# Kernel optimization log

Measured on AMD Instinct MI355X. Metric: run time of the kernel, lower is better.

The kernel has to match this reference:

```python
import jax, jax.numpy as jnp
import numpy as np

N_NODES = 50000
N_EDGES = 1600000
N_GRAPHS = 512
IN_DIM = 384
HID = 128


def gcn_conv(x, W, b, src, dst, n_nodes):
    # PyG GCNConv: h = W^T x, then propagate with sym norm over A + I (self-loops).
    h = x @ W  # [N, out]
    # self-loops
    loop = jnp.arange(n_nodes, dtype=src.dtype)
    s = jnp.concatenate([src, loop])
    d = jnp.concatenate([dst, loop])
    ones = jnp.ones(s.shape[0], dtype=h.dtype)
    deg = jax.ops.segment_sum(ones, d, num_segments=n_nodes)  # in-degree incl self-loop
    dis = jnp.where(deg > 0, jax.lax.rsqrt(deg), 0.0)
    norm = dis[s] * dis[d]  # [E+N]
    msg = h[s] * norm[:, None]  # gather + scale
    out = jax.ops.segment_sum(msg, d, num_segments=n_nodes)  # scatter-add
    return out + b


def global_mean_pool(x, batch, num_graphs):
    sums = jax.ops.segment_sum(x, batch, num_segments=num_graphs)
    cnt = jax.ops.segment_sum(jnp.ones(x.shape[0], dtype=x.dtype), batch, num_segments=num_graphs)
    return sums / jnp.maximum(cnt, 1.0)[:, None]


def setup_inputs() -> dict:
    key = jax.random.key(0)
    ks = jax.random.split(key, 12)
    x = jax.random.normal(ks[0], (N_NODES, IN_DIM), dtype=jnp.float32)
    edge_index = jax.random.randint(ks[1], (2, N_EDGES), 0, N_NODES, dtype=jnp.int64 if jax.config.jax_enable_x64 else jnp.int32)
    batch = jnp.sort(jax.random.randint(ks[2], (N_NODES,), 0, N_GRAPHS, dtype=jnp.int32))
    def glorot(k, shape):
        lim = float(np.sqrt(6.0 / (shape[0] + shape[1])))
        return jax.random.uniform(k, shape, jnp.float32, -lim, lim)
    return {
        "x": x,
        "edge_index": edge_index,
        "batch": batch,
        "W1": glorot(ks[3], (IN_DIM, HID)),
        "b1": jnp.zeros((HID,), jnp.float32),
        "W2": glorot(ks[4], (HID, HID)),
        "b2": jnp.zeros((HID,), jnp.float32),
        "Wl1": glorot(ks[5], (HID, HID // 2)),
        "bl1": jnp.zeros((HID // 2,), jnp.float32),
        "Wl2": glorot(ks[6], (HID // 2, 5)),
        "bl2": jnp.zeros((5,), jnp.float32),
    }


def reference(x, edge_index, batch, W1, b1, W2, b2, Wl1, bl1, Wl2, bl2):
    src, dst = edge_index[0], edge_index[1]
    n = x.shape[0]
    h = jax.nn.relu(gcn_conv(x, W1, b1, src, dst, n))
    h = jax.nn.relu(gcn_conv(h, W2, b2, src, dst, n))
    g = global_mean_pool(h, batch, N_GRAPHS)  # [G, HID]
    g = jax.nn.relu(g @ Wl1 + bl1)
    return jax.nn.sigmoid(g @ Wl2 + bl2)  # [G, 5]
```

## Files before the change

kernel.cpp:

```cpp
#include <hip/hip_runtime.h>
#include <hip/hip_bf16.h>
#include <string.h>

#define HID 128
#define NGRAPH 512
#define IN_DIM 384

typedef __attribute__((ext_vector_type(2))) float f32x2;

__device__ __forceinline__ float bf2f(unsigned short u) {
    unsigned int x = ((unsigned int)u) << 16;
    float f; __builtin_memcpy(&f, &x, 4); return f;
}
__device__ __forceinline__ unsigned short f2bf(float f) {
    unsigned int b; __builtin_memcpy(&b, &f, 4);
    unsigned int r = (b + 0x7FFFu + ((b >> 16) & 1u)) >> 16;
    return (unsigned short)r;
}

__global__ void deg_kernel(const int* __restrict__ dst, int* __restrict__ deg, int E) {
    int e = blockIdx.x * blockDim.x + threadIdx.x;
    if (e < E) atomicAdd(&deg[dst[e]], 1);
}

__global__ void dis_kernel(const int* __restrict__ deg, float* __restrict__ dis, int n) {
    int v = blockIdx.x * blockDim.x + threadIdx.x;
    if (v < n) dis[v] = rsqrtf((float)(deg[v] + 1));
}

__global__ __launch_bounds__(256) void scan_part(const int* __restrict__ deg, int* __restrict__ row,
                                                 int* __restrict__ blockSums, int n) {
    __shared__ int ts[256];
    const int b = blockIdx.x, t = threadIdx.x;
    const int base = b * 1024 + t * 4;
    int v0 = (base + 0 < n) ? deg[base + 0] : 0;
    int v1 = (base + 1 < n) ? deg[base + 1] : 0;
    int v2 = (base + 2 < n) ? deg[base + 2] : 0;
    int v3 = (base + 3 < n) ? deg[base + 3] : 0;
    const int s = v0 + v1 + v2 + v3;
    ts[t] = s;
    __syncthreads();
    for (int off = 1; off < 256; off <<= 1) {
        int x = (t >= off) ? ts[t - off] : 0;
        __syncthreads();
        ts[t] += x;
        __syncthreads();
    }
    int p = ts[t] - s;
    if (base + 0 < n) { row[base + 0] = p; p += v0; }
    if (base + 1 < n) { row[base + 1] = p; p += v1; }
    if (base + 2 < n) { row[base + 2] = p; p += v2; }
    if (base + 3 < n) { row[base + 3] = p; }
    if (t == 255) blockSums[b] = ts[255];
}

__global__ void scan_tops(int* __restrict__ blockSums, int nb) {
    if (threadIdx.x == 0 && blockIdx.x == 0) {
        int acc = 0;
        for (int i = 0; i < nb; i++) { int v = blockSums[i]; blockSums[i] = acc; acc += v; }
    }
}

__global__ __launch_bounds__(256) void scan_add(int* __restrict__ row, int* __restrict__ cursor,
                                                const int* __restrict__ blockSums, int n, int E) {
    const int b = blockIdx.x, t = threadIdx.x;
    const int off = blockSums[b];
    const int base = b * 1024 + t * 4;
#pragma unroll
    for (int j = 0; j < 4; j++) {
        int i = base + j;
        if (i < n) { int v = row[i] + off; row[i] = v; cursor[i] = v; }
    }
    if (b == 0 && t == 0) row[n] = E;
}

__global__ void fill_kernel(const int* __restrict__ src, const int* __restrict__ dst,
                            int* __restrict__ cursor, unsigned short* __restrict__ csr16,
                            int E, int lo, int hi) {
    int e = blockIdx.x * blockDim.x + threadIdx.x;
    if (e < E) {
        const int d = dst[e];
        if (d >= lo && d < hi) {
            int pos = atomicAdd(&cursor[d], 1);
            csr16[pos] = (unsigned short)src[e];
        }
    }
}

template <int K, bool BF16IN>
__global__ __launch_bounds__(256) void gemm_tile(const void* __restrict__ Xv,
                                                 const float* __restrict__ W,
                                                 const float* __restrict__ dis,
                                                 unsigned int* __restrict__ out8, int n) {
    constexpr int KC = 32;
    __shared__ float asT[KC][68];
    __shared__ float bs[KC * HID];
    const int t = threadIdx.x;
    const int tx = t & 31;
    const int ty = t >> 5;
    const int row0 = blockIdx.x * 64;

    float4 acc[8];
#pragma unroll
    for (int j = 0; j < 8; j++) acc[j] = make_float4(0.f, 0.f, 0.f, 0.f);

    const int ar = t >> 3;
    const int af = t & 7;

    for (int k0 = 0; k0 < K; k0 += KC) {
#pragma unroll
        for (int half = 0; half < 2; half++) {
            const int r = ar + half * 32;
            const int gr = row0 + r;
            float4 a = make_float4(0.f, 0.f, 0.f, 0.f);
            if (gr < n) {
                if constexpr (BF16IN) {
                    const ushort4 u = *(const ushort4*)((const unsigned short*)Xv + (long)gr * K + k0 + af * 4);
                    a.x = bf2f(u.x); a.y = bf2f(u.y); a.z = bf2f(u.z); a.w = bf2f(u.w);
                } else {
                    a = *(const float4*)((const float*)Xv + (long)gr * K + k0 + af * 4);
                }
            }
            asT[af * 4 + 0][r] = a.x;
            asT[af * 4 + 1][r] = a.y;
            asT[af * 4 + 2][r] = a.z;
            asT[af * 4 + 3][r] = a.w;
        }
        {
            const float4* wp = (const float4*)&W[(long)k0 * HID];
            float4* bp = (float4*)bs;
#pragma unroll
            for (int i = 0; i < 4; i++) bp[t + i * 256] = wp[t + i * 256];
        }
        __syncthreads();
#pragma unroll 8
        for (int kk = 0; kk < KC; kk++) {
            const float4 a0 = *(const float4*)&asT[kk][ty * 8];
            const float4 a1 = *(const float4*)&asT[kk][ty * 8 + 4];
            const float4 b  = *(const float4*)&bs[kk * HID + tx * 4];
            acc[0].x = fmaf(a0.x, b.x, acc[0].x); acc[0].y = fmaf(a0.x, b.y, acc[0].y);
            acc[0].z = fmaf(a0.x, b.z, acc[0].z); acc[0].w = fmaf(a0.x, b.w, acc[0].w);
            acc[1].x = fmaf(a0.y, b.x, acc[1].x); acc[1].y = fmaf(a0.y, b.y, acc[1].y);
            acc[1].z = fmaf(a0.y, b.z, acc[1].z); acc[1].w = fmaf(a0.y, b.w, acc[1].w);
            acc[2].x = fmaf(a0.z, b.x, acc[2].x); acc[2].y = fmaf(a0.z, b.y, acc[2].y);
            acc[2].z = fmaf(a0.z, b.z, acc[2].z); acc[2].w = fmaf(a0.z, b.w, acc[2].w);
            acc[3].x = fmaf(a0.w, b.x, acc[3].x); acc[3].y = fmaf(a0.w, b.y, acc[3].y);
            acc[3].z = fmaf(a0.w, b.z, acc[3].z); acc[3].w = fmaf(a0.w, b.w, acc[3].w);
            acc[4].x = fmaf(a1.x, b.x, acc[4].x); acc[4].y = fmaf(a1.x, b.y, acc[4].y);
            acc[4].z = fmaf(a1.x, b.z, acc[4].z); acc[4].w = fmaf(a1.x, b.w, acc[4].w);
            acc[5].x = fmaf(a1.y, b.x, acc[5].x); acc[5].y = fmaf(a1.y, b.y, acc[5].y);
            acc[5].z = fmaf(a1.y, b.z, acc[5].z); acc[5].w = fmaf(a1.y, b.w, acc[5].w);
            acc[6].x = fmaf(a1.z, b.x, acc[6].x); acc[6].y = fmaf(a1.z, b.y, acc[6].y);
            acc[6].z = fmaf(a1.z, b.z, acc[6].z); acc[6].w = fmaf(a1.z, b.w, acc[6].w);
            acc[7].x = fmaf(a1.w, b.x, acc[7].x); acc[7].y = fmaf(a1.w, b.y, acc[7].y);
            acc[7].z = fmaf(a1.w, b.z, acc[7].z); acc[7].w = fmaf(a1.w, b.w, acc[7].w);
        }
        __syncthreads();
    }

#pragma unroll
    for (int j = 0; j < 8; j++) {
        const int v = row0 + ty * 8 + j;
        if (v < n) {
            const float s = dis[v] * 8.0f;
            int w01 = __builtin_amdgcn_cvt_pk_fp8_f32(acc[j].x * s, acc[j].y * s, 0, false);
            int w   = __builtin_amdgcn_cvt_pk_fp8_f32(acc[j].z * s, acc[j].w * s, w01, true);
            out8[(long)v * (HID / 4) + tx] = (unsigned int)w;
        }
    }
}

template <bool POOL>
__global__ __launch_bounds__(256) void agg_kernel(const unsigned char* __restrict__ hs8,
                                                  const unsigned short* __restrict__ csr16,
                                                  const int* __restrict__ row,
                                                  const float* __restrict__ dis,
                                                  const float* __restrict__ bias,
                                                  const int* __restrict__ batch,
                                                  unsigned int* __restrict__ buf,
                                                  float* __restrict__ sums,
                                                  int* __restrict__ cnt, int n) {
    const int v = blockIdx.x * 4 + (threadIdx.x >> 6);
    if (v >= n) return;
    const int lane = threadIdx.x & 63;
    const int sub = lane >> 3;
    const int lc  = lane & 7;

    const int rs = row[v];
    const int re = row[v + 1];

    float acc[16];
#pragma unroll
    for (int i = 0; i < 16; i++) acc[i] = 0.f;

    for (int base = rs; base < re; base += 32) {
        uint4 w[4];
        int vld[4];
#pragma unroll
        for (int p = 0; p < 4; p++) {
            const int pe = base + p * 8;
            if (pe < re) {
                const int ei = pe + sub;
                const int idx = __builtin_nontemporal_load(&csr16[(ei < re) ? ei : (re - 1)]);
                w[p] = *(const uint4*)&hs8[(long)idx * HID + (lc << 4)];
                vld[p] = (ei < re);
            } else {
                w[p] = make_uint4(0u, 0u, 0u, 0u);
                vld[p] = 0;
            }
        }
#pragma unroll
        for (int p = 0; p < 4; p++) {
            if (vld[p]) {
                const uint4 ww = w[p];
                f32x2 u;
                u = __builtin_amdgcn_cvt_pk_f32_fp8(ww.x, false); acc[0]  += u.x; acc[1]  += u.y;
                u = __builtin_amdgcn_cvt_pk_f32_fp8(ww.x, true);  acc[2]  += u.x; acc[3]  += u.y;
                u = __builtin_amdgcn_cvt_pk_f32_fp8(ww.y, false); acc[4]  += u.x; acc[5]  += u.y;
                u = __builtin_amdgcn_cvt_pk_f32_fp8(ww.y, true);  acc[6]  += u.x; acc[7]  += u.y;
                u = __builtin_amdgcn_cvt_pk_f32_fp8(ww.z, false); acc[8]  += u.x; acc[9]  += u.y;
                u = __builtin_amdgcn_cvt_pk_f32_fp8(ww.z, true);  acc[10] += u.x; acc[11] += u.y;
                u = __builtin_amdgcn_cvt_pk_f32_fp8(ww.w, false); acc[12] += u.x; acc[13] += u.y;
                u = __builtin_amdgcn_cvt_pk_f32_fp8(ww.w, true);  acc[14] += u.x; acc[15] += u.y;
            }
        }
    }

#pragma unroll
    for (int i = 0; i < 16; i++) {
        acc[i] += __shfl_xor(acc[i], 8, 64);
        acc[i] += __shfl_xor(acc[i], 16, 64);
        acc[i] += __shfl_xor(acc[i], 32, 64);
    }

    const int col = (lc << 4) + (sub << 1);
    const unsigned short selfw = *(const unsigned short*)&hs8[(long)v * HID + col];
    f32x2 sf = __builtin_amdgcn_cvt_pk_f32_fp8((unsigned int)selfw, false);
    const float sx = acc[(sub << 1) + 0] + sf.x;
    const float sy = acc[(sub << 1) + 1] + sf.y;
    const float dv = dis[v] * 0.125f;
    const float rx = fmaxf(fmaf(dv, sx, bias[col]), 0.f);
    const float ry = fmaxf(fmaf(dv, sy, bias[col + 1]), 0.f);
    if (POOL) {
        const int g = batch[v];
        unsafeAtomicAdd(&sums[g * HID + col], rx);
        unsafeAtomicAdd(&sums[g * HID + col + 1], ry);
        if (lane == 0) atomicAdd(&cnt[g], 1);
    } else {
        const unsigned int pk = (unsigned int)f2bf(rx) | ((unsigned int)f2bf(ry) << 16);
        buf[(long)v * (HID / 2) + (col >> 1)] = pk;
    }
}

__global__ __launch_bounds__(64) void mlp_kernel(const float* __restrict__ sums,
                                                 const int* __restrict__ cnt,
                                                 const float* __restrict__ Wl1,
                                                 const float* __restrict__ bl1,
                                                 const float* __restrict__ Wl2,
                                                 const float* __restrict__ bl2,
                                                 float* __restrict__ out) {
    const int g = blockIdx.x, t = threadIdx.x;
    __shared__ float mean[HID];
    __shared__ float hid[64];
    const float c = fmaxf((float)cnt[g], 1.0f);
    mean[t] = sums[g * HID + t] / c;
    mean[t + 64] = sums[g * HID + 64 + t] / c;
    __syncthreads();
    float acc = bl1[t];
#pragma unroll 4
    for (int k = 0; k < HID; k++) acc = fmaf(mean[k], Wl1[k * 64 + t], acc);
    hid[t] = fmaxf(acc, 0.f);
    __syncthreads();
    if (t < 5) {
        float a = bl2[t];
#pragma unroll 4
        for (int k = 0; k < 64; k++) a = fmaf(hid[k], Wl2[k * 5 + t], a);
        out[g * 5 + t] = 1.f / (1.f + expf(-a));
    }
}

extern "C" void kernel_launch(void* const* d_in, const int* in_sizes, int n_in,
                              void* d_out, int out_size, void* d_ws, size_t ws_size,
                              hipStream_t stream) {
    const float* x   = (const float*)d_in[0];
    const int* ei    = (const int*)d_in[1];
    const int* batch = (const int*)d_in[2];
    const float* W1  = (const float*)d_in[3];
    const float* b1  = (const float*)d_in[4];
    const float* W2  = (const float*)d_in[5];
    const float* b2  = (const float*)d_in[6];
    const float* Wl1 = (const float*)d_in[7];
    const float* bl1 = (const float*)d_in[8];
    const float* Wl2 = (const float*)d_in[9];
    const float* bl2 = (const float*)d_in[10];
    float* out = (float*)d_out;

    const int n = in_sizes[0] / IN_DIM;
    const int E = in_sizes[1] / 2;
    const int* src = ei;
    const int* dst = ei + E;

    char* ws = (char*)d_ws;
    size_t off = 0;
    auto alloc = [&](size_t bytes) {
        void* p = ws + off;
        off = (off + bytes + 255) & ~(size_t)255;
        return p;
    };
    int*   deg       = (int*)alloc((size_t)n * 4);
    float* dis       = (float*)alloc((size_t)n * 4);
    int*   row       = (int*)alloc((size_t)(n + 1) * 4);
    int*   cursor    = (int*)alloc((size_t)n * 4);
    unsigned short* csr16 = (unsigned short*)alloc((size_t)E * 2);
    int*   blockSums = (int*)alloc(256 * 4);
    unsigned char* hs8 = (unsigned char*)alloc((size_t)n * HID);
    unsigned int* buf1 = (unsigned int*)alloc((size_t)n * HID * 2);
    float* sums = (float*)alloc((size_t)NGRAPH * HID * 4);
    int*   cnt  = (int*)alloc((size_t)NGRAPH * 4);
    (void)ws_size;

    const int nb = (n + 1023) / 1024;
    const int gemmBlocks = (n + 63) / 64;
    const int aggBlocks  = (n + 3) / 4;
    const int edgeBlocks = (E + 255) / 256;

    hipMemsetAsync(deg, 0, (size_t)n * 4, stream);
    deg_kernel<<<edgeBlocks, 256, 0, stream>>>(dst, deg, E);
    dis_kernel<<<(n + 255) / 256, 256, 0, stream>>>(deg, dis, n);
    scan_part<<<nb, 256, 0, stream>>>(deg, row, blockSums, n);
    scan_tops<<<1, 64, 0, stream>>>(blockSums, nb);
    scan_add<<<nb, 256, 0, stream>>>(row, cursor, blockSums, n, E);
    {
        const int step = (n + 3) / 4;
        for (int k = 0; k < 4; k++) {
            const int lo = k * step;
            const int hi = (k == 3) ? n : (lo + step);
            fill_kernel<<<edgeBlocks, 256, 0, stream>>>(src, dst, cursor, csr16, E, lo, hi);
        }
    }

    gemm_tile<IN_DIM, false><<<gemmBlocks, 256, 0, stream>>>(x, W1, dis, (unsigned int*)hs8, n);
    agg_kernel<false><<<aggBlocks, 256, 0, stream>>>(hs8, csr16, row, dis, b1, batch,
                                                     buf1, nullptr, nullptr, n);

    gemm_tile<HID, true><<<gemmBlocks, 256, 0, stream>>>(buf1, W2, dis, (unsigned int*)hs8, n);
    hipMemsetAsync(sums, 0, (size_t)NGRAPH * HID * 4, stream);
    hipMemsetAsync(cnt, 0, (size_t)NGRAPH * 4, stream);
    agg_kernel<true><<<aggBlocks, 256, 0, stream>>>(hs8, csr16, row, dis, b2, batch,
                                                    nullptr, sums, cnt, n);

    mlp_kernel<<<NGRAPH, 64, 0, stream>>>(sums, cnt, Wl1, bl1, Wl2, bl2, out);
}
```

Before: 586.0 us.

## Fuse CSR scan into one block and overlap edge fill with first GEMM

Replaces the three-kernel prefix scan and the separate dis kernel with a single 1024-thread block that scans degrees and writes row, cursor and dis together. Merges the four range-partitioned CSR fill launches and the first GEMM into one grid, interleaving GEMM blocks among fill blocks so the compute-bound and atomic-bound work can share the GPU. It also combines the two pooling memsets into one. This cuts launch count and serialization, but a single-block scan with per-thread sequential chunks reads memory non-coalesced and uses only one CU. The fill sweeps are no longer ordered relative to each other.

```diff
diff --git a/kernel.cpp b/kernel.cpp
--- a/kernel.cpp
+++ b/kernel.cpp
@@ -18,87 +18,18 @@
     return (unsigned short)r;
 }
 
-__global__ void deg_kernel(const int* __restrict__ dst, int* __restrict__ deg, int E) {
-    int e = blockIdx.x * blockDim.x + threadIdx.x;
-    if (e < E) atomicAdd(&deg[dst[e]], 1);
-}
-
-__global__ void dis_kernel(const int* __restrict__ deg, float* __restrict__ dis, int n) {
-    int v = blockIdx.x * blockDim.x + threadIdx.x;
-    if (v < n) dis[v] = rsqrtf((float)(deg[v] + 1));
-}
-
-__global__ __launch_bounds__(256) void scan_part(const int* __restrict__ deg, int* __restrict__ row,
-                                                 int* __restrict__ blockSums, int n) {
-    __shared__ int ts[256];
-    const int b = blockIdx.x, t = threadIdx.x;
-    const int base = b * 1024 + t * 4;
-    int v0 = (base + 0 < n) ? deg[base + 0] : 0;
-    int v1 = (base + 1 < n) ? deg[base + 1] : 0;
-    int v2 = (base + 2 < n) ? deg[base + 2] : 0;
-    int v3 = (base + 3 < n) ? deg[base + 3] : 0;
-    const int s = v0 + v1 + v2 + v3;
-    ts[t] = s;
-    __syncthreads();
-    for (int off = 1; off < 256; off <<= 1) {
-        int x = (t >= off) ? ts[t - off] : 0;
-        __syncthreads();
-        ts[t] += x;
-        __syncthreads();
-    }
-    int p = ts[t] - s;
-    if (base + 0 < n) { row[base + 0] = p; p += v0; }
-    if (base + 1 < n) { row[base + 1] = p; p += v1; }
-    if (base + 2 < n) { row[base + 2] = p; p += v2; }
-    if (base + 3 < n) { row[base + 3] = p; }
-    if (t == 255) blockSums[b] = ts[255];
-}
-
-__global__ void scan_tops(int* __restrict__ blockSums, int nb) {
-    if (threadIdx.x == 0 && blockIdx.x == 0) {
-        int acc = 0;
-        for (int i = 0; i < nb; i++) { int v = blockSums[i]; blockSums[i] = acc; acc += v; }
-    }
-}
-
-__global__ __launch_bounds__(256) void scan_add(int* __restrict__ row, int* __restrict__ cursor,
-                                                const int* __restrict__ blockSums, int n, int E) {
-    const int b = blockIdx.x, t = threadIdx.x;
-    const int off = blockSums[b];
-    const int base = b * 1024 + t * 4;
-#pragma unroll
-    for (int j = 0; j < 4; j++) {
-        int i = base + j;
-        if (i < n) { int v = row[i] + off; row[i] = v; cursor[i] = v; }
-    }
-    if (b == 0 && t == 0) row[n] = E;
-}
-
-__global__ void fill_kernel(const int* __restrict__ src, const int* __restrict__ dst,
-                            int* __restrict__ cursor, unsigned short* __restrict__ csr16,
-                            int E, int lo, int hi) {
-    int e = blockIdx.x * blockDim.x + threadIdx.x;
-    if (e < E) {
-        const int d = dst[e];
-        if (d >= lo && d < hi) {
-            int pos = atomicAdd(&cursor[d], 1);
-            csr16[pos] = (unsigned short)src[e];
-        }
-    }
-}
-
 template <int K, bool BF16IN>
-__global__ __launch_bounds__(256) void gemm_tile(const void* __restrict__ Xv,
-                                                 const float* __restrict__ W,
-                                                 const float* __restrict__ dis,
-                                                 unsigned int* __restrict__ out8, int n) {
+__device__ __forceinline__ void gemm_body(float (*asT)[68], float* bs,
+                                          const void* __restrict__ Xv,
+                                          const float* __restrict__ W,
+                                          const float* __restrict__ dis,
+                                          unsigned int* __restrict__ out8,
+                                          int n, int blk) {
     constexpr int KC = 32;
-    __shared__ float asT[KC][68];
-    __shared__ float bs[KC * HID];
     const int t = threadIdx.x;
     const int tx = t & 31;
     const int ty = t >> 5;
-    const int row0 = blockIdx.x * 64;
+    const int row0 = blk * 64;
 
     float4 acc[8];
 #pragma unroll
@@ -168,6 +99,84 @@
             out8[(long)v * (HID / 4) + tx] = (unsigned int)w;
         }
     }
+}
+
+__global__ void deg_kernel(const int* __restrict__ dst, int* __restrict__ deg, int E) {
+    int e = blockIdx.x * blockDim.x + threadIdx.x;
+    if (e < E) atomicAdd(&deg[dst[e]], 1);
+}
+
+__global__ __launch_bounds__(1024) void scan_fused(const int* __restrict__ deg,
+                                                   int* __restrict__ row,
+                                                   int* __restrict__ cursor,
+                                                   float* __restrict__ dis,
+                                                   int n, int E) {
+    __shared__ int ts[1024];
+    const int t = threadIdx.x;
+    const int CH = (n + 1023) >> 10;
+    const int lo = t * CH;
+    const int hi = min(lo + CH, n);
+    int s = 0;
+    for (int i = lo; i < hi; ++i) s += deg[i];
+    ts[t] = s;
+    __syncthreads();
+    for (int off = 1; off < 1024; off <<= 1) {
+        int x = (t >= off) ? ts[t - off] : 0;
+        __syncthreads();
+        ts[t] += x;
+        __syncthreads();
+    }
+    int p = ts[t] - s;
+    for (int i = lo; i < hi; ++i) {
+        const int d = deg[i];
+        row[i] = p; cursor[i] = p;
+        dis[i] = rsqrtf((float)(d + 1));
+        p += d;
+    }
+    if (t == 0) row[n] = E;
+}
+
+__global__ __launch_bounds__(256) void gemm1_fill(const float* __restrict__ X,
+                                                  const float* __restrict__ W,
+                                                  const float* __restrict__ dis,
+                                                  unsigned int* __restrict__ out8, int n,
+                                                  const int* __restrict__ src,
+                                                  const int* __restrict__ dst,
+                                                  int* __restrict__ cursor,
+                                                  unsigned short* __restrict__ csr16,
+                                                  int E, int gemmBlocks, int stride,
+                                                  int edgeBlocks, int step) {
+    __shared__ float asT[32][68];
+    __shared__ float bs[32 * HID];
+    const int bid = blockIdx.x;
+    const bool isG = ((bid % stride) == 0) && ((bid / stride) < gemmBlocks);
+    if (isG) {
+        gemm_body<IN_DIM, false>(asT, bs, X, W, dis, out8, n, bid / stride);
+    } else {
+        const int gBefore = min((bid + stride - 1) / stride, gemmBlocks);
+        const int fillIdx = bid - gBefore;
+        const int sweep  = fillIdx / edgeBlocks;
+        const int within = fillIdx - sweep * edgeBlocks;
+        const int e = within * 256 + (int)threadIdx.x;
+        if (e < E) {
+            const int d = dst[e];
+            const int lo = sweep * step;
+            const int hi = (sweep == 3) ? n : (lo + step);
+            if (d >= lo && d < hi) {
+                int pos = atomicAdd(&cursor[d], 1);
+                csr16[pos] = (unsigned short)src[e];
+            }
+        }
+    }
+}
+
+__global__ __launch_bounds__(256) void gemm_tile2(const unsigned short* __restrict__ X,
+                                                  const float* __restrict__ W,
+                                                  const float* __restrict__ dis,
+                                                  unsigned int* __restrict__ out8, int n) {
+    __shared__ float asT[32][68];
+    __shared__ float bs[32 * HID];
+    gemm_body<HID, true>(asT, bs, X, W, dis, out8, n, blockIdx.x);
 }
 
 template <bool POOL>
@@ -312,40 +321,35 @@
     int*   row       = (int*)alloc((size_t)(n + 1) * 4);
     int*   cursor    = (int*)alloc((size_t)n * 4);
     unsigned short* csr16 = (unsigned short*)alloc((size_t)E * 2);
-    int*   blockSums = (int*)alloc(256 * 4);
     unsigned char* hs8 = (unsigned char*)alloc((size_t)n * HID);
     unsigned int* buf1 = (unsigned int*)alloc((size_t)n * HID * 2);
     float* sums = (float*)alloc((size_t)NGRAPH * HID * 4);
     int*   cnt  = (int*)alloc((size_t)NGRAPH * 4);
     (void)ws_size;
 
-    const int nb = (n + 1023) / 1024;
     const int gemmBlocks = (n + 63) / 64;
     const int aggBlocks  = (n + 3) / 4;
     const int edgeBlocks = (E + 255) / 256;
+    const int step       = (n + 3) / 4;
+    const int fusedTot   = gemmBlocks + 4 * edgeBlocks;
+    const int stride     = max(1, fusedTot / gemmBlocks);
 
     hipMemsetAsync(deg, 0, (size_t)n * 4, stream);
+    hipMemsetAsync(sums, 0, (size_t)NGRAPH * HID * 4 + (size_t)NGRAPH * 4, stream);
+
     deg_kernel<<<edgeBlocks, 256, 0, stream>>>(dst, deg, E);
-    dis_kernel<<<(n + 255) / 256, 256, 0, stream>>>(deg, dis, n);
-    scan_part<<<nb, 256, 0, stream>>>(deg, row, blockSums, n);
-    scan_tops<<<1, 64, 0, stream>>>(blockSums, nb);
-    scan_add<<<nb, 256, 0, stream>>>(row, cursor, blockSums, n, E);
-    {
-        const int step = (n + 3) / 4;
-        for (int k = 0; k < 4; k++) {
-            const int lo = k * step;
-            const int hi = (k == 3) ? n : (lo + step);
-            fill_kernel<<<edgeBlocks, 256, 0, stream>>>(src, dst, cursor, csr16, E, lo, hi);
-        }
-    }
-
-    gemm_tile<IN_DIM, false><<<gemmBlocks, 256, 0, stream>>>(x, W1, dis, (unsigned int*)hs8, n);
+
+    scan_fused<<<1, 1024, 0, stream>>>(deg, row, cursor, dis, n, E);
+
+    gemm1_fill<<<fusedTot, 256, 0, stream>>>(x, W1, dis, (unsigned int*)hs8, n,
+                                             src, dst, cursor, csr16, E,
+                                             gemmBlocks, stride, edgeBlocks, step);
+
     agg_kernel<false><<<aggBlocks, 256, 0, stream>>>(hs8, csr16, row, dis, b1, batch,
                                                      buf1, nullptr, nullptr, n);
 
-    gemm_tile<HID, true><<<gemmBlocks, 256, 0, stream>>>(buf1, W2, dis, (unsigned int*)hs8, n);
-    hipMemsetAsync(sums, 0, (size_t)NGRAPH * HID * 4, stream);
-    hipMemsetAsync(cnt, 0, (size_t)NGRAPH * 4, stream);
+    gemm_tile2<<<gemmBlocks, 256, 0, stream>>>((const unsigned short*)buf1, W2, dis,
+                                               (unsigned int*)hs8, n);
     agg_kernel<true><<<aggBlocks, 256, 0, stream>>>(hs8, csr16, row, dis, b2, batch,
                                                     nullptr, sums, cnt, n);
 
```

After: 2.014 ms. 244% more time.
